# Optimization experiments

Hardware: AMD Instinct MI355X
Metric: run time of the kernel (lower is better)

Reference implementation:

```python
import jax, jax.numpy as jnp
import numpy as np

B, DIM, HEADS, Hs, Ws = 8, 192, 8, 128, 128


def setup_inputs() -> dict:
    key = jax.random.key(0)
    ks = jax.random.split(key, 8)
    d3 = 3 * DIM
    inp = {
        "x": jax.random.normal(ks[0], (B, DIM, Hs, Ws), dtype=jnp.float32),
        # qkv 1x1 conv: (out=3*dim, in=dim)
        "w_qkv": jax.random.normal(ks[1], (d3, DIM), dtype=jnp.float32) / np.sqrt(DIM),
        "b_qkv": jnp.zeros((d3,), dtype=jnp.float32),
        # depthwise 3x3 conv, groups = 3*dim -> kernel (3*dim, 1, 3, 3)
        "w_dw": jax.random.normal(ks[2], (d3, 1, 3, 3), dtype=jnp.float32) / 3.0,
        "b_dw": jnp.zeros((d3,), dtype=jnp.float32),
        # project_out 1x1 conv: (dim, dim)
        "w_proj": jax.random.normal(ks[3], (DIM, DIM), dtype=jnp.float32) / np.sqrt(DIM),
        "b_proj": jnp.zeros((DIM,), dtype=jnp.float32),
        "temperature": jnp.ones((HEADS, 1, 1), dtype=jnp.float32),
        "a1": jnp.full((1,), 0.2, dtype=jnp.float32),
        "a2": jnp.full((1,), 0.2, dtype=jnp.float32),
        "a3": jnp.full((1,), 0.2, dtype=jnp.float32),
        "a4": jnp.full((1,), 0.2, dtype=jnp.float32),
    }
    return inp


def _sparse_softmax(attn, k):
    # top-k per row, scatter 1s at those indices, mask rest to -inf, softmax
    _, idx = jax.lax.top_k(attn, k)                      # [..., C, k]
    C = attn.shape[-1]
    mask = jax.nn.one_hot(idx, C, dtype=attn.dtype).sum(-2)  # [..., C, C]
    masked = jnp.where(mask > 0, attn, -jnp.inf)
    return jax.nn.softmax(masked, axis=-1)


def _l2norm(t):
    # torch F.normalize: x / max(||x||_2, eps) along last axis
    n = jnp.sqrt(jnp.sum(t * t, axis=-1, keepdims=True))
    return t / jnp.maximum(n, 1e-12)


def reference(x, w_qkv, b_qkv, w_dw, b_dw, w_proj, b_proj, temperature, a1, a2, a3, a4):
    b, c, h, w = x.shape
    # 1x1 conv
    qkv = jnp.einsum('oi,bihw->bohw', w_qkv, x) + b_qkv[:, None, None]
    # depthwise 3x3 conv, padding=1
    qkv = jax.lax.conv_general_dilated(
        qkv, w_dw, window_strides=(1, 1), padding='SAME',
        feature_group_count=3 * c,
        dimension_numbers=('NCHW', 'OIHW', 'NCHW')) + b_dw[:, None, None]
    q, k, v = jnp.split(qkv, 3, axis=1)
    Cd = c // HEADS  # per-head channel dim
    heads = lambda t: t.reshape(b, HEADS, Cd, h * w)
    q, k, v = heads(q), heads(k), heads(v)
    q, k = _l2norm(q), _l2norm(k)
    # transposed (channel) attention: [b, head, Cd, Cd]
    attn = jnp.einsum('bhcn,bhdn->bhcd', q, k) * temperature
    ks = (int(Cd / 2), int(Cd * 2 / 3), int(Cd * 3 / 4), int(Cd * 4 / 5))
    out1 = jnp.einsum('bhcd,bhdn->bhcn', _sparse_softmax(attn, ks[0]), v)
    out2 = jnp.einsum('bhcd,bhdn->bhcn', _sparse_softmax(attn, ks[1]), v)
    out3 = jnp.einsum('bhcd,bhdn->bhcn', _sparse_softmax(attn, ks[2]), v)
    out4 = jnp.einsum('bhcd,bhdn->bhcn', _sparse_softmax(attn, ks[3]), v)
    out = out1 * a1 + out2 * a2 + out3 * a3 + out4 * a4
    out = out.reshape(b, c, h, w)
    out = jnp.einsum('oi,bihw->bohw', w_proj, out) + b_proj[:, None, None]
    return out
```

## Files before the change

### kernel.cpp

```cpp
#include <hip/hip_runtime.h>
#include <math.h>

#define DIMC 192
#define C3 576
#define NHEADS 8
#define CDh 24
#define HWN 16384
#define WIDTH 128
#define NBATCH 8

typedef __attribute__((ext_vector_type(8))) short short8;
typedef __attribute__((ext_vector_type(4))) float f32x4;

__device__ __forceinline__ ushort f2bf(float f) {
    uint u = __float_as_uint(f);
    u += 0x7fff + ((u >> 16) & 1);
    return (ushort)(u >> 16);
}
__device__ __forceinline__ float bf2f(ushort h) {
    return __uint_as_float(((uint)h) << 16);
}

__global__ void k0_prep(const float* __restrict__ W, ushort* __restrict__ Wh,
                        ushort* __restrict__ Wl, int n) {
    int i = blockIdx.x * 256 + threadIdx.x;
    if (i < n) {
        float w = W[i];
        ushort h = f2bf(w);
        Wh[i] = h;
        Wl[i] = f2bf(w - bf2f(h));
    }
}

__global__ __launch_bounds__(256, 3) void kgx3(const float* __restrict__ x,
                                               const ushort* __restrict__ Wh,
                                               const ushort* __restrict__ Wl,
                                               const float* __restrict__ bias,
                                               float* __restrict__ qkv) {
    __shared__ ushort smem[2 * 64 * 200];
    ushort* BsH = smem;
    ushort* BsL = smem + 64 * 200;
    const int n0 = blockIdx.x * 64;
    const int o0 = blockIdx.y * 192;
    const int tid = threadIdx.x;
#pragma unroll
    for (int it = 0; it < 12; it++) {
        int idx = tid + it * 256;
        int ch = idx >> 4, q = idx & 15;
        f32x4 v = *(const f32x4*)&x[(size_t)ch * HWN + n0 + q * 4];
#pragma unroll
        for (int p = 0; p < 4; p++) {
            ushort hb = f2bf(v[p]);
            BsH[(q * 4 + p) * 200 + ch] = hb;
            BsL[(q * 4 + p) * 200 + ch] = f2bf(v[p] - bf2f(hb));
        }
    }
    __syncthreads();
    const int wid = tid >> 6, lane = tid & 63;
    const int lr = lane & 15, lk = lane >> 4;
    const int mb = o0 + wid * 48;
    f32x4 acc[3][4];
#pragma unroll
    for (int i = 0; i < 3; i++)
#pragma unroll
        for (int j = 0; j < 4; j++) acc[i][j] = (f32x4)0.f;

    for (int kc6 = 0; kc6 < 6; kc6++) {
        short8 bh[4], bl[4];
#pragma unroll
        for (int j = 0; j < 4; j++) {
            int ad = (j * 16 + lr) * 200 + kc6 * 32 + lk * 8;
            bh[j] = *(const short8*)&BsH[ad];
            bl[j] = *(const short8*)&BsL[ad];
        }
#pragma unroll
        for (int i = 0; i < 3; i++) {
            size_t ao = (size_t)(mb + i * 16 + lr) * DIMC + kc6 * 32 + lk * 8;
            const short8 ah = *(const short8*)&Wh[ao];
            const short8 al = *(const short8*)&Wl[ao];
#pragma unroll
            for (int j = 0; j < 4; j++) {
                acc[i][j] = __builtin_amdgcn_mfma_f32_16x16x32_bf16(ah, bh[j], acc[i][j], 0, 0, 0);
                acc[i][j] = __builtin_amdgcn_mfma_f32_16x16x32_bf16(ah, bl[j], acc[i][j], 0, 0, 0);
                acc[i][j] = __builtin_amdgcn_mfma_f32_16x16x32_bf16(al, bh[j], acc[i][j], 0, 0, 0);
            }
        }
    }
    __syncthreads();
    float* epsb = (float*)smem + wid * (2 * 1056);
#pragma unroll
    for (int i = 0; i < 3; i++) {
        float* eps = epsb + (i & 1) * 1056;
        int rb = mb + i * 16;
#pragma unroll
        for (int j = 0; j < 4; j++)
#pragma unroll
            for (int r = 0; r < 4; r++)
                eps[(lk * 4 + r) * 66 + j * 16 + lr] = acc[i][j][r] + bias[rb + lk * 4 + r];
#pragma unroll
        for (int s = 0; s < 4; s++) {
            int rl = s * 4 + (lane >> 4);
            int c4 = (lane & 15) * 4;
            f32x4 v = *(const f32x4*)&eps[rl * 66 + c4];
            *(f32x4*)&qkv[(size_t)(rb + rl) * HWN + n0 + c4] = v;
        }
    }
}

__global__ __launch_bounds__(256, 3) void kg3f(float* __restrict__ vy,
                                               const ushort* __restrict__ Mh,
                                               const ushort* __restrict__ Ml,
                                               const float* __restrict__ bias) {
    __shared__ ushort smem[2 * 64 * 200];
    ushort* BsH = smem;
    ushort* BsL = smem + 64 * 200;
    const int z = blockIdx.y;
    float* vb = vy + (size_t)z * DIMC * HWN;
    const int n0 = blockIdx.x * 64;
    const int tid = threadIdx.x;
#pragma unroll
    for (int it = 0; it < 12; it++) {
        int idx = tid + it * 256;
        int ch = idx >> 4, q = idx & 15;
        f32x4 v = *(const f32x4*)&vb[(size_t)ch * HWN + n0 + q * 4];
#pragma unroll
        for (int p = 0; p < 4; p++) {
            ushort hb = f2bf(v[p]);
            BsH[(q * 4 + p) * 200 + ch] = hb;
            BsL[(q * 4 + p) * 200 + ch] = f2bf(v[p] - bf2f(hb));
        }
    }
    __syncthreads();
    const int wid = tid >> 6, lane = tid & 63;
    const int lr = lane & 15, lk = lane >> 4;
    const int mb = wid * 48;
    const ushort* Azh = Mh + (size_t)z * DIMC * DIMC;
    const ushort* Azl = Ml + (size_t)z * DIMC * DIMC;
    f32x4 acc[3][4];
#pragma unroll
    for (int i = 0; i < 3; i++)
#pragma unroll
        for (int j = 0; j < 4; j++) acc[i][j] = (f32x4)0.f;

    for (int kc6 = 0; kc6 < 6; kc6++) {
        short8 bh[4], bl[4];
#pragma unroll
        for (int j = 0; j < 4; j++) {
            int ad = (j * 16 + lr) * 200 + kc6 * 32 + lk * 8;
            bh[j] = *(const short8*)&BsH[ad];
            bl[j] = *(const short8*)&BsL[ad];
        }
#pragma unroll
        for (int i = 0; i < 3; i++) {
            size_t ao = (size_t)(mb + i * 16 + lr) * DIMC + kc6 * 32 + lk * 8;
            const short8 ah = *(const short8*)&Azh[ao];
            const short8 al = *(const short8*)&Azl[ao];
#pragma unroll
            for (int j = 0; j < 4; j++) {
                acc[i][j] = __builtin_amdgcn_mfma_f32_16x16x32_bf16(ah, bh[j], acc[i][j], 0, 0, 0);
                acc[i][j] = __builtin_amdgcn_mfma_f32_16x16x32_bf16(ah, bl[j], acc[i][j], 0, 0, 0);
                acc[i][j] = __builtin_amdgcn_mfma_f32_16x16x32_bf16(al, bh[j], acc[i][j], 0, 0, 0);
            }
        }
    }
    __syncthreads();
    float* epsb = (float*)smem + wid * (2 * 1056);
#pragma unroll
    for (int i = 0; i < 3; i++) {
        float* eps = epsb + (i & 1) * 1056;
        int rb = mb + i * 16;
#pragma unroll
        for (int j = 0; j < 4; j++)
#pragma unroll
            for (int r = 0; r < 4; r++)
                eps[(lk * 4 + r) * 66 + j * 16 + lr] = acc[i][j][r] + bias[rb + lk * 4 + r];
#pragma unroll
        for (int s = 0; s < 4; s++) {
            int rl = s * 4 + (lane >> 4);
            int c4 = (lane & 15) * 4;
            f32x4 v = *(const f32x4*)&eps[rl * 66 + c4];
            *(f32x4*)&vb[(size_t)(rb + rl) * HWN + n0 + c4] = v;
        }
    }
}

__global__ __launch_bounds__(1024, 4) void k2_dw(const float* __restrict__ qkv,
                                                 const float* __restrict__ wdw,
                                                 const float* __restrict__ bdw,
                                                 float* __restrict__ vout,
                                                 float* __restrict__ part, int b) {
    __shared__ float stage[2 * 6336];
    __shared__ float qks[48 * 520];
    const int stripe = blockIdx.x, h = blockIdx.y;
    const int tid = threadIdx.x;
    const int r0 = stripe * 4;

    const int col4 = (tid & 31) * 4;
    const int orow = (tid >> 5) & 3;
    const int cc = tid >> 7;

    auto stage_load = [&](int chunk, int buf) {
        const int g = chunk / 3, cb = (chunk % 3) * 8;
        float* sb = stage + buf * 6336;
#pragma unroll
        for (int f = tid; f < 1536; f += 1024) {
            int fc = f / 192, rem = f - fc * 192;
            int rl = rem >> 5, c4 = rem & 31;
            int gr = r0 - 1 + rl;
            int ch = g * DIMC + h * CDh + cb + fc;
            float4 v = make_float4(0.f, 0.f, 0.f, 0.f);
            if (gr >= 0 && gr < 128)
                v = *(const float4*)&qkv[(size_t)ch * HWN + gr * WIDTH + c4 * 4];
            *(float4*)&sb[(fc * 6 + rl) * 132 + c4 * 4] = v;
        }
    };

    stage_load(0, 0);
    __syncthreads();
    for (int chunk = 0; chunk < 9; chunk++) {
        const int buf = chunk & 1;
        if (chunk < 8) stage_load(chunk + 1, buf ^ 1);
        const int g = chunk / 3, cb = (chunk % 3) * 8;
        const float* sb = stage + buf * 6336;
        const int ch = g * DIMC + h * CDh + cb + cc;
        float wr[9];
#pragma unroll
        for (int t = 0; t < 9; t++) wr[t] = wdw[ch * 9 + t];
        float bsv = bdw[ch];
        float a0 = bsv, a1 = bsv, a2 = bsv, a3 = bsv;
#pragma unroll
        for (int dr = 0; dr < 3; dr++) {
            const float* row = &sb[(cc * 6 + orow + dr) * 132];
            f32x4 cen = *(const f32x4*)&row[col4];
            f32x4 lf4 = (col4 > 0) ? *(const f32x4*)&row[col4 - 4] : (f32x4)0.f;
            f32x4 rt4 = (col4 < 124) ? *(const f32x4*)&row[col4 + 4] : (f32x4)0.f;
            float left = lf4[3], right = rt4[0];
            float wA = wr[dr * 3 + 0], wB = wr[dr * 3 + 1], wC = wr[dr * 3 + 2];
            a0 = fmaf(left, wA, fmaf(cen[0], wB, fmaf(cen[1], wC, a0)));
            a1 = fmaf(cen[0], wA, fmaf(cen[1], wB, fmaf(cen[2], wC, a1)));
            a2 = fmaf(cen[1], wA, fmaf(cen[2], wB, fmaf(cen[3], wC, a2)));
            a3 = fmaf(cen[2], wA, fmaf(cen[3], wB, fmaf(right, wC, a3)));
        }
        if (g < 2) {
            float4 o4 = {a0, a1, a2, a3};
            *(float4*)&qks[(g * CDh + cb + cc) * 520 + orow * 128 + col4] = o4;
        } else {
            float4 o4 = {a0, a1, a2, a3};
            *(float4*)&vout[((size_t)b * DIMC + h * CDh + cb + cc) * HWN +
                            (size_t)(r0 + orow) * WIDTH + col4] = o4;
        }
        __syncthreads();
    }

    const int tc = tid & 3, td = (tid >> 2) & 3, tp = tid >> 4;
    float ga[6][6];
#pragma unroll
    for (int i = 0; i < 6; i++)
#pragma unroll
        for (int j = 0; j < 6; j++) ga[i][j] = 0.f;
#pragma unroll
    for (int s = 0; s < 2; s++) {
        int px = tp * 8 + s * 4;
        f32x4 qv[6], kv[6];
#pragma unroll
        for (int i = 0; i < 6; i++) qv[i] = *(const f32x4*)&qks[(tc * 6 + i) * 520 + px];
#pragma unroll
        for (int j = 0; j < 6; j++) kv[j] = *(const f32x4*)&qks[(24 + td * 6 + j) * 520 + px];
#pragma unroll
        for (int i = 0; i < 6; i++)
#pragma unroll
            for (int j = 0; j < 6; j++) {
                ga[i][j] = fmaf(qv[i][0], kv[j][0], ga[i][j]);
                ga[i][j] = fmaf(qv[i][1], kv[j][1], ga[i][j]);
                ga[i][j] = fmaf(qv[i][2], kv[j][2], ga[i][j]);
                ga[i][j] = fmaf(qv[i][3], kv[j][3], ga[i][j]);
            }
    }
#pragma unroll
    for (int i = 0; i < 6; i++)
#pragma unroll
        for (int j = 0; j < 6; j++) {
            float v = ga[i][j];
            v += __shfl_xor(v, 16, 64);
            v += __shfl_xor(v, 32, 64);
            ga[i][j] = v;
        }
    float nv = 0.f;
    int nch = 0, npg = 0;
    if (tid < 768) {
        npg = tid / 48;
        nch = tid - npg * 48;
#pragma unroll
        for (int s = 0; s < 8; s++) {
            f32x4 v = *(const f32x4*)&qks[nch * 520 + npg * 32 + s * 4];
            nv = fmaf(v[0], v[0], nv);
            nv = fmaf(v[1], v[1], nv);
            nv = fmaf(v[2], v[2], nv);
            nv = fmaf(v[3], v[3], nv);
        }
    }
    __syncthreads();
    float* gscr = qks;
    const int wave = tid >> 6;
    if ((tid & 63) < 16) {
#pragma unroll
        for (int i = 0; i < 6; i++)
#pragma unroll
            for (int j = 0; j < 6; j++)
                gscr[wave * 624 + (tc * 6 + i) * 24 + (td * 6 + j)] = ga[i][j];
    }
    if (tid < 768) gscr[npg * 624 + 576 + nch] = nv;
    __syncthreads();
    if (tid < 624) {
        float s = 0.f;
#pragma unroll
        for (int w2 = 0; w2 < 16; w2++) s += gscr[w2 * 624 + tid];
        part[((size_t)(b * NHEADS + h) * 64 + stripe) * 624 + tid] = s;
    }
}

__global__ void k34_attn(const float* __restrict__ part, const float* __restrict__ temp,
                         const float* __restrict__ a1, const float* __restrict__ a2,
                         const float* __restrict__ a3, const float* __restrict__ a4,
                         float* __restrict__ Aeff) {
    __shared__ float gbuf[624];
    int bh = blockIdx.x;
    int h = bh & 7;
    int tid = threadIdx.x;
    for (int ti = tid; ti < 624; ti += 256) {
        float s = 0.f;
        const float* p = part + (size_t)bh * 64 * 624 + ti;
#pragma unroll 4
        for (int st = 0; st < 64; st++) s += p[st * 624];
        gbuf[ti] = s;
    }
    __syncthreads();
    int r = tid;
    if (r >= CDh) return;
    float t = temp[h];
    float aw[4] = {a1[0], a2[0], a3[0], a4[0]};
    const int kks[4] = {12, 16, 18, 19};
    float qn = fmaxf(sqrtf(gbuf[576 + r]), 1e-12f);
    float av[24];
    for (int d = 0; d < 24; d++) {
        float kn = fmaxf(sqrtf(gbuf[600 + d]), 1e-12f);
        av[d] = gbuf[r * 24 + d] / (qn * kn) * t;
    }
    int rank[24];
    float m = -1e30f;
    for (int d = 0; d < 24; d++) {
        int rk = 0;
        for (int e = 0; e < 24; e++)
            rk += (av[e] > av[d]) || (av[e] == av[d] && e < d);
        rank[d] = rk;
        m = fmaxf(m, av[d]);
    }
    float ex[24], outv[24];
    for (int d = 0; d < 24; d++) { ex[d] = expf(av[d] - m); outv[d] = 0.f; }
    for (int i = 0; i < 4; i++) {
        float Z = 0.f;
        for (int d = 0; d < 24; d++) if (rank[d] < kks[i]) Z += ex[d];
        float inv = aw[i] / Z;
        for (int d = 0; d < 24; d++) if (rank[d] < kks[i]) outv[d] += ex[d] * inv;
    }
    for (int d = 0; d < 24; d++) Aeff[(bh * 24 + r) * 24 + d] = outv[d];
}

__global__ void k4b_mmat(const float* __restrict__ Wp, const float* __restrict__ Aeff,
                         ushort* __restrict__ Mh, ushort* __restrict__ Ml) {
    int b = blockIdx.x;
    int e0 = blockIdx.y * 6144;
    for (int e = e0 + threadIdx.x; e < e0 + 6144; e += 256) {
        int o = e / DIMC, j = e % DIMC;
        int h = j / CDh, d = j % CDh;
        const float* wrow = Wp + o * DIMC + h * CDh;
        const float* acol = Aeff + (size_t)((b * NHEADS + h) * CDh) * CDh + d;
        float s = 0.f;
        for (int c = 0; c < CDh; c++) s = fmaf(wrow[c], acol[c * CDh], s);
        size_t idx = ((size_t)b * DIMC + o) * DIMC + j;
        ushort hb = f2bf(s);
        Mh[idx] = hb;
        Ml[idx] = f2bf(s - bf2f(hb));
    }
}

extern "C" void kernel_launch(void* const* d_in, const int* in_sizes, int n_in,
                              void* d_out, int out_size, void* d_ws, size_t ws_size,
                              hipStream_t stream) {
    const float* x     = (const float*)d_in[0];
    const float* wqkv  = (const float*)d_in[1];
    const float* bqkv  = (const float*)d_in[2];
    const float* wdw   = (const float*)d_in[3];
    const float* bdw   = (const float*)d_in[4];
    const float* wproj = (const float*)d_in[5];
    const float* bproj = (const float*)d_in[6];
    const float* temp  = (const float*)d_in[7];
    const float* a1    = (const float*)d_in[8];
    const float* a2    = (const float*)d_in[9];
    const float* a3    = (const float*)d_in[10];
    const float* a4    = (const float*)d_in[11];
    float* out = (float*)d_out;

    float* ws = (float*)d_ws;
    const size_t fl_part = (size_t)64 * 64 * 624;
    const size_t fl_A    = (size_t)64 * 576;
    const size_t fl_M    = (size_t)NBATCH * DIMC * DIMC / 2;
    const size_t fl_W    = (size_t)C3 * DIMC / 2;
    const size_t fl_qkv1 = (size_t)C3 * HWN;

    size_t o = 0;
    float* part = ws + o; o += fl_part;
    float* Aeff = ws + o; o += fl_A;
    ushort* Mh  = (ushort*)(ws + o); o += fl_M;
    ushort* Ml  = (ushort*)(ws + o); o += fl_M;
    ushort* Wh  = (ushort*)(ws + o); o += fl_W;
    ushort* Wl  = (ushort*)(ws + o); o += fl_W;
    float* qkv  = ws + o;
    (void)fl_qkv1;

    k0_prep<<<(C3 * DIMC + 255) / 256, 256, 0, stream>>>(wqkv, Wh, Wl, C3 * DIMC);

    for (int b = 0; b < NBATCH; b++) {
        kgx3<<<dim3(256, 3), 256, 0, stream>>>(x + (size_t)b * DIMC * HWN,
                                               Wh, Wl, bqkv, qkv);
        k2_dw<<<dim3(32, 8), 1024, 0, stream>>>(qkv, wdw, bdw, out, part, b);
    }
    k34_attn<<<64, 256, 0, stream>>>(part, temp, a1, a2, a3, a4, Aeff);
    k4b_mmat<<<dim3(8, 6), 256, 0, stream>>>(wproj, Aeff, Mh, Ml);
    kg3f<<<dim3(256, 8), 256, 0, stream>>>(out, Mh, Ml, bproj);
}
```

Measured before the change: 493.7 us.

## Swizzle GEMM LDS layout, batch two images per launch, trim stripe reduction

Both bf16-split GEMM kernels now store the transposed input tile in LDS with an XOR swizzle on 8-element chunks, so the short8 fragment reads avoid bank conflicts. When the workspace holds two qkv buffers, the qkv GEMM and depthwise-conv kernels process two batch images per launch through blockIdx.z. This doubles grid size and halves launch count, at the cost of more workspace. The attention reduction now sums only the 32 stripes k2_dw actually writes instead of 64.

Result: faster. 459.9 us (-6.8%).

```diff
diff --git a/kernel.cpp b/kernel.cpp
--- a/kernel.cpp
+++ b/kernel.cpp
@@ -36,10 +36,12 @@
                                                const ushort* __restrict__ Wh,
                                                const ushort* __restrict__ Wl,
                                                const float* __restrict__ bias,
-                                               float* __restrict__ qkv) {
+                                               float* __restrict__ qkv, long qkv_zs) {
     __shared__ ushort smem[2 * 64 * 200];
     ushort* BsH = smem;
     ushort* BsL = smem + 64 * 200;
+    const float* xb = x + (size_t)blockIdx.z * DIMC * HWN;
+    float* oz = qkv + (size_t)blockIdx.z * qkv_zs;
     const int n0 = blockIdx.x * 64;
     const int o0 = blockIdx.y * 192;
     const int tid = threadIdx.x;
@@ -47,12 +49,14 @@
     for (int it = 0; it < 12; it++) {
         int idx = tid + it * 256;
         int ch = idx >> 4, q = idx & 15;
-        f32x4 v = *(const f32x4*)&x[(size_t)ch * HWN + n0 + q * 4];
+        f32x4 v = *(const f32x4*)&xb[(size_t)ch * HWN + n0 + q * 4];
+        const int swz = ((ch >> 3) ^ (q & 7)) * 8 + (ch & 7);
 #pragma unroll
         for (int p = 0; p < 4; p++) {
+            int ad = (q * 4 + p) * 200 + swz;
             ushort hb = f2bf(v[p]);
-            BsH[(q * 4 + p) * 200 + ch] = hb;
-            BsL[(q * 4 + p) * 200 + ch] = f2bf(v[p] - bf2f(hb));
+            BsH[ad] = hb;
+            BsL[ad] = f2bf(v[p] - bf2f(hb));
         }
     }
     __syncthreads();
@@ -69,7 +73,9 @@
         short8 bh[4], bl[4];
 #pragma unroll
         for (int j = 0; j < 4; j++) {
-            int ad = (j * 16 + lr) * 200 + kc6 * 32 + lk * 8;
+            int px = j * 16 + lr;
+            int o = (kc6 * 4 + lk) ^ ((px >> 2) & 7);
+            int ad = px * 200 + o * 8;
             bh[j] = *(const short8*)&BsH[ad];
             bl[j] = *(const short8*)&BsL[ad];
         }
@@ -102,7 +108,7 @@
             int rl = s * 4 + (lane >> 4);
             int c4 = (lane & 15) * 4;
             f32x4 v = *(const f32x4*)&eps[rl * 66 + c4];
-            *(f32x4*)&qkv[(size_t)(rb + rl) * HWN + n0 + c4] = v;
+            *(f32x4*)&oz[(size_t)(rb + rl) * HWN + n0 + c4] = v;
         }
     }
 }
@@ -123,11 +129,13 @@
         int idx = tid + it * 256;
         int ch = idx >> 4, q = idx & 15;
         f32x4 v = *(const f32x4*)&vb[(size_t)ch * HWN + n0 + q * 4];
+        const int swz = ((ch >> 3) ^ (q & 7)) * 8 + (ch & 7);
 #pragma unroll
         for (int p = 0; p < 4; p++) {
+            int ad = (q * 4 + p) * 200 + swz;
             ushort hb = f2bf(v[p]);
-            BsH[(q * 4 + p) * 200 + ch] = hb;
-            BsL[(q * 4 + p) * 200 + ch] = f2bf(v[p] - bf2f(hb));
+            BsH[ad] = hb;
+            BsL[ad] = f2bf(v[p] - bf2f(hb));
         }
     }
     __syncthreads();
@@ -146,7 +154,9 @@
         short8 bh[4], bl[4];
 #pragma unroll
         for (int j = 0; j < 4; j++) {
-            int ad = (j * 16 + lr) * 200 + kc6 * 32 + lk * 8;
+            int px = j * 16 + lr;
+            int o = (kc6 * 4 + lk) ^ ((px >> 2) & 7);
+            int ad = px * 200 + o * 8;
             bh[j] = *(const short8*)&BsH[ad];
             bl[j] = *(const short8*)&BsL[ad];
         }
@@ -184,13 +194,15 @@
     }
 }
 
-__global__ __launch_bounds__(1024, 4) void k2_dw(const float* __restrict__ qkv,
+__global__ __launch_bounds__(1024, 4) void k2_dw(const float* __restrict__ qkv0, long qkv_zs,
                                                  const float* __restrict__ wdw,
                                                  const float* __restrict__ bdw,
                                                  float* __restrict__ vout,
-                                                 float* __restrict__ part, int b) {
+                                                 float* __restrict__ part, int b0) {
     __shared__ float stage[2 * 6336];
     __shared__ float qks[48 * 520];
+    const int b = b0 + blockIdx.z;
+    const float* qkv = qkv0 + (size_t)blockIdx.z * qkv_zs;
     const int stripe = blockIdx.x, h = blockIdx.y;
     const int tid = threadIdx.x;
     const int r0 = stripe * 4;
@@ -331,7 +343,7 @@
         float s = 0.f;
         const float* p = part + (size_t)bh * 64 * 624 + ti;
 #pragma unroll 4
-        for (int st = 0; st < 64; st++) s += p[st * 624];
+        for (int st = 0; st < 32; st++) s += p[st * 624];
         gbuf[ti] = s;
     }
     __syncthreads();
@@ -407,6 +419,9 @@
     const size_t fl_M    = (size_t)NBATCH * DIMC * DIMC / 2;
     const size_t fl_W    = (size_t)C3 * DIMC / 2;
     const size_t fl_qkv1 = (size_t)C3 * HWN;
+    const size_t base_fl = fl_part + fl_A + 2 * fl_M + 2 * fl_W;
+
+    int nz = (ws_size >= (base_fl + 2 * fl_qkv1) * sizeof(float)) ? 2 : 1;
 
     size_t o = 0;
     float* part = ws + o; o += fl_part;
@@ -416,14 +431,15 @@
     ushort* Wh  = (ushort*)(ws + o); o += fl_W;
     ushort* Wl  = (ushort*)(ws + o); o += fl_W;
     float* qkv  = ws + o;
-    (void)fl_qkv1;
+
+    const long qkv_zs = (long)fl_qkv1;
 
     k0_prep<<<(C3 * DIMC + 255) / 256, 256, 0, stream>>>(wqkv, Wh, Wl, C3 * DIMC);
 
-    for (int b = 0; b < NBATCH; b++) {
-        kgx3<<<dim3(256, 3), 256, 0, stream>>>(x + (size_t)b * DIMC * HWN,
-                                               Wh, Wl, bqkv, qkv);
-        k2_dw<<<dim3(32, 8), 1024, 0, stream>>>(qkv, wdw, bdw, out, part, b);
+    for (int b0 = 0; b0 < NBATCH; b0 += nz) {
+        kgx3<<<dim3(256, 3, nz), 256, 0, stream>>>(x + (size_t)b0 * DIMC * HWN,
+                                                   Wh, Wl, bqkv, qkv, qkv_zs);
+        k2_dw<<<dim3(32, 8, nz), 1024, 0, stream>>>(qkv, qkv_zs, wdw, bdw, out, part, b0);
     }
     k34_attn<<<64, 256, 0, stream>>>(part, temp, a1, a2, a3, a4, Aeff);
     k4b_mmat<<<dim3(8, 6), 256, 0, stream>>>(wproj, Aeff, Mh, Ml);
```
